# Optimization experiments

Measured on AMD Instinct MI355X. Metric: run time of the kernel, lower is better.

The kernel has to match this reference:

```python
import jax, jax.numpy as jnp
import numpy as np

N_NODES = 100000
N_EDGES = 3200000
N_GRAPHS = 256
IN_DIM = 128
HID = 64
K = 3


def setup_inputs() -> dict:
    key = jax.random.key(0)
    ks = jax.random.split(key, 10)
    x = jax.random.normal(ks[0], (N_NODES, IN_DIM), dtype=jnp.float32)
    edge_index = jax.random.randint(ks[1], (2, N_EDGES), 0, N_NODES, dtype=jnp.int64)
    batch = jnp.sort(jax.random.randint(ks[2], (N_NODES,), 0, N_GRAPHS, dtype=jnp.int64))
    # ChebConv k-order weights: list of Linear(in, out) -> stacked [K, in, out]
    s1 = 1.0 / np.sqrt(IN_DIM)
    s2 = 1.0 / np.sqrt(HID)
    W1 = jax.random.uniform(ks[3], (K, IN_DIM, HID), jnp.float32, -s1, s1)
    b1 = jax.random.uniform(ks[4], (HID,), jnp.float32, -s1, s1)
    W2 = jax.random.uniform(ks[5], (K, HID, HID), jnp.float32, -s2, s2)
    b2 = jax.random.uniform(ks[6], (HID,), jnp.float32, -s2, s2)
    Wfc = jax.random.uniform(ks[7], (HID, 1), jnp.float32, -s2, s2)
    bfc = jax.random.uniform(ks[8], (1,), jnp.float32, -s2, s2)
    return {"x": x, "edge_index": edge_index, "batch": batch,
            "W1": W1, "b1": b1, "W2": W2, "b2": b2, "Wfc": Wfc, "bfc": bfc}


def _cheb_conv(x, src, dst, edge_w, W, b):
    # PyG ChebConv, sym normalization, lambda_max=2 => L_hat has zero diagonal
    # and off-diagonal -D^{-1/2} A D^{-1/2} (edge_w precomputed, negative).
    n = x.shape[0]
    def lhat(v):  # (L_hat v)_i = sum_{edges j->i} edge_w * v_j
        return jax.ops.segment_sum(edge_w[:, None] * v[src], dst, num_segments=n)
    Tx0 = x
    Tx1 = lhat(Tx0)
    Tx2 = 2.0 * lhat(Tx1) - Tx0
    return Tx0 @ W[0] + Tx1 @ W[1] + Tx2 @ W[2] + b


def reference(x, edge_index, batch, W1, b1, W2, b2, Wfc, bfc):
    src, dst = edge_index[0], edge_index[1]
    n = x.shape[0]
    # degree on row (source), sym normalization
    deg = jax.ops.segment_sum(jnp.ones_like(src, dtype=x.dtype), src, num_segments=n)
    dinv = jnp.where(deg > 0, jax.lax.rsqrt(jnp.maximum(deg, 1.0)), 0.0)
    edge_w = -dinv[src] * dinv[dst]  # scaled Laplacian off-diagonal weights

    h = jax.nn.relu(_cheb_conv(x, src, dst, edge_w, W1, b1))
    h = jax.nn.relu(_cheb_conv(h, src, dst, edge_w, W2, b2))

    # global mean pool over graphs
    sums = jax.ops.segment_sum(h, batch, num_segments=N_GRAPHS)
    counts = jax.ops.segment_sum(jnp.ones((n,), dtype=h.dtype), batch, num_segments=N_GRAPHS)
    pooled = sums / jnp.maximum(counts, 1.0)[:, None]

    return (pooled @ Wfc + bfc).squeeze(-1)  # [N_GRAPHS]
```

## Files before the change

kernel.cpp:

```cpp
#include <hip/hip_runtime.h>
#include <hip/hip_fp16.h>
#include <cstdint>
#include <cstddef>

static constexpr int NN = 100000;
static constexpr int NE = 3200000;
static constexpr int NG = 256;
static constexpr int NBK = (NN + 127) / 128;
static constexpr int EPB = NE / 256;
static constexpr int GB_BATCH = (NN + 255) / 256;
static constexpr int GB_PREPW = (192 * 128 + 192 * 64 + 255) / 256;
static constexpr int GB_HIST = 256;

typedef _Float16 h8 __attribute__((ext_vector_type(8)));
typedef float f4v __attribute__((ext_vector_type(4)));

__device__ __forceinline__ void atomAddF(float* p, float v) {
  unsafeAtomicAdd(p, v);
}
__device__ __forceinline__ float h2f(__half h) { return __half2float(h); }

__global__ void k_detect(const int* __restrict__ ei, int* __restrict__ flag) {
  if (threadIdx.x == 0 && blockIdx.x == 0) {
    int nz = 0;
    for (int i = 0; i < 64; ++i) nz += (ei[2 * i + 1] != 0) ? 1 : 0;
    *flag = (nz == 0) ? 1 : 0;
  }
}

__device__ __forceinline__ int ld_idx(const void* raw, int f, int i) {
  return f ? (int)((const long long*)raw)[i] : ((const int*)raw)[i];
}

__global__ __launch_bounds__(256) void k_front(const void* __restrict__ bat,
                                               const void* __restrict__ ei,
                                               const int* __restrict__ flag,
                                               const float* __restrict__ W1,
                                               const float* __restrict__ W2,
                                               int* __restrict__ b32,
                                               int* __restrict__ gcnt,
                                               __half* __restrict__ BtX,
                                               __half* __restrict__ BtH2,
                                               int* __restrict__ sCnt,
                                               int* __restrict__ dCnt,
                                               int* __restrict__ hsBlk,
                                               int* __restrict__ hdBlk) {
  __shared__ int sh[2 * NBK];
  int b = blockIdx.x;
  int t = threadIdx.x;
  if (b < GB_BATCH) {
    int* cnt = sh;
    cnt[t] = 0;
    int blk0 = b * 256;
    int f = *flag;
    int g0 = ld_idx(bat, f, blk0);
    __syncthreads();
    int i = blk0 + t;
    if (i < NN) {
      int g = ld_idx(bat, f, i);
      b32[i] = g;
      atomicAdd(&cnt[g - g0], 1);
    }
    __syncthreads();
    if (cnt[t] > 0) atomicAdd(&gcnt[g0 + t], cnt[t]);
  } else if (b < GB_BATCH + GB_PREPW) {
    int u = (b - GB_BATCH) * 256 + t;
    if (u < 192 * 128) {
      int n = u >> 7, k = u & 127;
      float v;
      if (n < 64)       v = W1[k * 64 + n] - W1[16384 + k * 64 + n];
      else if (n < 128) v = W1[8192 + k * 64 + (n - 64)];
      else              v = W1[16384 + k * 64 + (n - 128)];
      BtX[n * 128 + k] = __float2half_rn(v);
    } else if (u < 192 * 128 + 192 * 64) {
      int u2 = u - 192 * 128;
      int n = u2 >> 6, k = u2 & 63;
      float v;
      if (n < 64)       v = W2[k * 64 + n] - W2[8192 + k * 64 + n];
      else if (n < 128) v = W2[4096 + k * 64 + (n - 64)];
      else              v = W2[8192 + k * 64 + (n - 128)];
      BtH2[n * 64 + k] = __float2half_rn(v);
    }
  } else {
    int hb = b - GB_BATCH - GB_PREPW;
    int* hs = sh;
    int* hd = sh + NBK;
    for (int i = t; i < NBK; i += 256) { hs[i] = 0; hd[i] = 0; }
    __syncthreads();
    int f = *flag;
    int e0 = hb * EPB;
    for (int e = e0 + t; e < e0 + EPB; e += 256) {
      int s = ld_idx(ei, f, e);
      int d = ld_idx(ei, f, NE + e);
      atomicAdd(&hs[s >> 7], 1);
      atomicAdd(&hd[d >> 7], 1);
    }
    __syncthreads();
    size_t hoff = (size_t)hb * NBK;
    for (int i = t; i < NBK; i += 256) {
      int a = hs[i], c = hd[i];
      hsBlk[hoff + i] = a;
      hdBlk[hoff + i] = c;
      if (a) atomicAdd(&sCnt[i], a);
      if (c) atomicAdd(&dCnt[i], c);
    }
  }
}

__global__ __launch_bounds__(1024) void k_scan(const int* __restrict__ sCnt,
                                               const int* __restrict__ dCnt,
                                               int* __restrict__ sBase,
                                               int* __restrict__ dBase,
                                               int* __restrict__ sCur,
                                               int* __restrict__ dCur) {
  __shared__ int sh1[1024], sh2[1024];
  int t = threadIdx.x;
  int v1 = (t < NBK) ? sCnt[t] : 0;
  int v2 = (t < NBK) ? dCnt[t] : 0;
  sh1[t] = v1; sh2[t] = v2;
  __syncthreads();
  for (int off = 1; off < 1024; off <<= 1) {
    int a1 = (t >= off) ? sh1[t - off] : 0;
    int a2 = (t >= off) ? sh2[t - off] : 0;
    __syncthreads();
    sh1[t] += a1; sh2[t] += a2;
    __syncthreads();
  }
  if (t <= NBK) {
    int b1 = sh1[t] - v1, b2 = sh2[t] - v2;
    sBase[t] = b1; dBase[t] = b2;
    if (t < NBK) { sCur[t] = b1; dCur[t] = b2; }
  }
}

__global__ __launch_bounds__(256) void k_scatter(const void* __restrict__ raw,
                                                 const int* __restrict__ flag,
                                                 const int* __restrict__ hsBlk,
                                                 const int* __restrict__ hdBlk,
                                                 int* __restrict__ sCur,
                                                 int* __restrict__ dCur,
                                                 int* __restrict__ srclist,
                                                 unsigned* __restrict__ elist) {
  __shared__ int hs[NBK], hd[NBK], cbS[NBK], cbD[NBK];
  int t = threadIdx.x;
  size_t hb = (size_t)blockIdx.x * NBK;
  for (int i = t; i < NBK; i += 256) {
    int c1 = hsBlk[hb + i];
    cbS[i] = c1 ? atomicAdd(&sCur[i], c1) : 0;
    int c2 = hdBlk[hb + i];
    cbD[i] = c2 ? atomicAdd(&dCur[i], c2) : 0;
    hs[i] = 0; hd[i] = 0;
  }
  __syncthreads();
  int f = *flag;
  int e0 = blockIdx.x * EPB;
  for (int e = e0 + t; e < e0 + EPB; e += 256) {
    int s = ld_idx(raw, f, e);
    int d = ld_idx(raw, f, NE + e);
    int bs = s >> 7, bd = d >> 7;
    int ls = atomicAdd(&hs[bs], 1);
    int ld2 = atomicAdd(&hd[bd], 1);
    srclist[cbS[bs] + ls] = s;
    elist[cbD[bd] + ld2] = (unsigned)s | ((unsigned)(d & 127) << 17);
  }
}

__global__ __launch_bounds__(256) void k_back(const int* __restrict__ sBase,
                                              const int* __restrict__ srclist,
                                              float* __restrict__ dinv,
                                              const int* __restrict__ dBase,
                                              const unsigned* __restrict__ elist,
                                              int* __restrict__ rowptr,
                                              int* __restrict__ adj) {
  __shared__ int cnt[128], sc[128], off[128], fill[128];
  int t = threadIdx.x;
  int bb = blockIdx.x;
  if (bb < NBK) {
    int b = bb;
    if (t < 128) cnt[t] = 0;
    __syncthreads();
    int e0 = sBase[b], e1 = sBase[b + 1];
    for (int i = e0 + t; i < e1; i += 256) atomicAdd(&cnt[srclist[i] & 127], 1);
    __syncthreads();
    if (t < 128) {
      int node = b * 128 + t;
      if (node < NN) {
        int c = cnt[t];
        dinv[node] = (c > 0) ? rsqrtf((float)c) : 0.f;
      }
    }
  } else {
    int b = bb - NBK;
    if (t < 128) { cnt[t] = 0; fill[t] = 0; }
    __syncthreads();
    int e0 = dBase[b], e1 = dBase[b + 1];
    for (int i = e0 + t; i < e1; i += 256) atomicAdd(&cnt[elist[i] >> 17], 1);
    __syncthreads();
    if (t < 128) sc[t] = cnt[t];
    __syncthreads();
    for (int o = 1; o < 128; o <<= 1) {
      int a = (t < 128 && t >= o) ? sc[t - o] : 0;
      __syncthreads();
      if (t < 128) sc[t] += a;
      __syncthreads();
    }
    if (t < 128) {
      off[t] = sc[t] - cnt[t];
      int node = b * 128 + t;
      if (node < NN) rowptr[node] = e0 + off[t];
    }
    if (b == NBK - 1 && t == 0) rowptr[NN] = e1;
    __syncthreads();
    for (int i = e0 + t; i < e1; i += 256) {
      unsigned w2 = elist[i];
      int l = (int)(w2 >> 17);
      int pos = atomicAdd(&fill[l], 1);
      adj[e0 + off[l] + pos] = (int)(w2 & 0x1FFFFu);
    }
  }
}

static constexpr int AW = 136;
__global__ __launch_bounds__(256) void k_gemm_x(const float* __restrict__ x,
                                                const __half* __restrict__ BtX,
                                                const float* __restrict__ dinv,
                                                __half* __restrict__ gV0,
                                                __half* __restrict__ gA1,
                                                __half* __restrict__ gU2s) {
  __shared__ __align__(16) _Float16 As[128 * AW];
  const int t = threadIdx.x;
  const int n0 = blockIdx.x * 128;
  {
    int i = t >> 1, q = t & 1;
    int row = n0 + i;
    _Float16* dst = As + i * AW + q * 64;
    if (row < NN) {
      const float* src = x + (size_t)row * 128 + q * 64;
#pragma unroll
      for (int c = 0; c < 64; c += 4) {
        float4 v = *reinterpret_cast<const float4*>(src + c);
        ushort4 u;
        u.x = __half_as_ushort(__float2half_rn(v.x));
        u.y = __half_as_ushort(__float2half_rn(v.y));
        u.z = __half_as_ushort(__float2half_rn(v.z));
        u.w = __half_as_ushort(__float2half_rn(v.w));
        *reinterpret_cast<ushort4*>(dst + c) = u;
      }
    } else {
#pragma unroll
      for (int c = 0; c < 64; c += 4)
        *reinterpret_cast<ushort4*>(dst + c) = make_ushort4(0, 0, 0, 0);
    }
  }
  __syncthreads();
  const int w = t >> 6, lane = t & 63;
  const int quad = lane >> 4, l = lane & 15;
  f4v acc[2][12];
#pragma unroll
  for (int mt = 0; mt < 2; ++mt)
#pragma unroll
    for (int nt = 0; nt < 12; ++nt) acc[mt][nt] = (f4v){0.f, 0.f, 0.f, 0.f};

#pragma unroll
  for (int ks = 0; ks < 4; ++ks) {
    int k0 = ks * 32 + quad * 8;
    h8 a0 = *reinterpret_cast<const h8*>(As + (w * 32 + l) * AW + k0);
    h8 a1 = *reinterpret_cast<const h8*>(As + (w * 32 + 16 + l) * AW + k0);
#pragma unroll
    for (int nt = 0; nt < 12; ++nt) {
      h8 b = *reinterpret_cast<const h8*>(BtX + (size_t)(nt * 16 + l) * 128 + k0);
      acc[0][nt] = __builtin_amdgcn_mfma_f32_16x16x32_f16(a0, b, acc[0][nt], 0, 0, 0);
      acc[1][nt] = __builtin_amdgcn_mfma_f32_16x16x32_f16(a1, b, acc[1][nt], 0, 0, 0);
    }
  }
#pragma unroll
  for (int mt = 0; mt < 2; ++mt) {
#pragma unroll
    for (int r = 0; r < 4; ++r) {
      int row = n0 + w * 32 + mt * 16 + quad * 4 + r;
      if (row < NN) {
        float dv = dinv[row];
#pragma unroll
        for (int nt2 = 0; nt2 < 4; ++nt2) {
          int col = nt2 * 16 + l;
          gV0[(size_t)row * 64 + col] = __float2half_rn(acc[mt][nt2][r]);
          gA1[(size_t)row * 64 + col] = __float2half_rn(acc[mt][4 + nt2][r]);
          gU2s[(size_t)row * 64 + col] = __float2half_rn(dv * acc[mt][8 + nt2][r]);
        }
      }
    }
  }
}

static constexpr int HW2 = 72;
__global__ __launch_bounds__(256) void k_gemm_h(const __half* __restrict__ gH1,
                                                const __half* __restrict__ BtH2,
                                                const float* __restrict__ dinv,
                                                __half* __restrict__ gV02,
                                                __half* __restrict__ gA2,
                                                __half* __restrict__ gB2s) {
  __shared__ __align__(16) _Float16 As[128 * HW2];
  const int t = threadIdx.x;
  const int n0 = blockIdx.x * 128;
  for (int c = t; c < 128 * 8; c += 256) {
    int row = c >> 3, seg = c & 7;
    int rowg = n0 + row;
    h8 v = (h8){0, 0, 0, 0, 0, 0, 0, 0};
    if (rowg < NN) v = *reinterpret_cast<const h8*>(gH1 + (size_t)rowg * 64 + seg * 8);
    *reinterpret_cast<h8*>(As + row * HW2 + seg * 8) = v;
  }
  __syncthreads();
  const int w = t >> 6, lane = t & 63;
  const int quad = lane >> 4, l = lane & 15;
  f4v acc[2][12];
#pragma unroll
  for (int mt = 0; mt < 2; ++mt)
#pragma unroll
    for (int nt = 0; nt < 12; ++nt) acc[mt][nt] = (f4v){0.f, 0.f, 0.f, 0.f};
#pragma unroll
  for (int ks = 0; ks < 2; ++ks) {
    int k0 = ks * 32 + quad * 8;
    h8 a0 = *reinterpret_cast<const h8*>(As + (w * 32 + l) * HW2 + k0);
    h8 a1 = *reinterpret_cast<const h8*>(As + (w * 32 + 16 + l) * HW2 + k0);
#pragma unroll
    for (int nt = 0; nt < 12; ++nt) {
      h8 b = *reinterpret_cast<const h8*>(BtH2 + (size_t)(nt * 16 + l) * 64 + k0);
      acc[0][nt] = __builtin_amdgcn_mfma_f32_16x16x32_f16(a0, b, acc[0][nt], 0, 0, 0);
      acc[1][nt] = __builtin_amdgcn_mfma_f32_16x16x32_f16(a1, b, acc[1][nt], 0, 0, 0);
    }
  }
#pragma unroll
  for (int mt = 0; mt < 2; ++mt) {
#pragma unroll
    for (int r = 0; r < 4; ++r) {
      int row = n0 + w * 32 + mt * 16 + quad * 4 + r;
      if (row < NN) {
        float dv = dinv[row];
#pragma unroll
        for (int nt2 = 0; nt2 < 4; ++nt2) {
          int col = nt2 * 16 + l;
          gV02[(size_t)row * 64 + col] = __float2half_rn(acc[mt][nt2][r]);
          gA2[(size_t)row * 64 + col] = __float2half_rn(acc[mt][4 + nt2][r]);
          gB2s[(size_t)row * 64 + col] = __float2half_rn(dv * acc[mt][8 + nt2][r]);
        }
      }
    }
  }
}

#define GATHER_SUM(tbl)                                                    \
  int p0 = rp[node], p1 = rp[node + 1];                                    \
  float a0 = 0.f, a1 = 0.f, a2 = 0.f, a3 = 0.f;                            \
  int p = p0;                                                              \
  int pA = (p0 + 3) & ~3;                                                  \
  if (pA > p1) pA = p1;                                                    \
  for (; p < pA; ++p) a0 += h2f(tbl[(size_t)adj[p] * 64 + d]);             \
  for (; p + 8 <= p1; p += 8) {                                            \
    int4 e0 = *reinterpret_cast<const int4*>(adj + p);                     \
    int4 e1 = *reinterpret_cast<const int4*>(adj + p + 4);                 \
    a0 += h2f(tbl[(size_t)e0.x * 64 + d]);                                 \
    a1 += h2f(tbl[(size_t)e0.y * 64 + d]);                                 \
    a2 += h2f(tbl[(size_t)e0.z * 64 + d]);                                 \
    a3 += h2f(tbl[(size_t)e0.w * 64 + d]);                                 \
    a0 += h2f(tbl[(size_t)e1.x * 64 + d]);                                 \
    a1 += h2f(tbl[(size_t)e1.y * 64 + d]);                                 \
    a2 += h2f(tbl[(size_t)e1.z * 64 + d]);                                 \
    a3 += h2f(tbl[(size_t)e1.w * 64 + d]);                                 \
  }                                                                        \
  if (p + 4 <= p1) {                                                       \
    int4 e = *reinterpret_cast<const int4*>(adj + p);                      \
    a0 += h2f(tbl[(size_t)e.x * 64 + d]);                                  \
    a1 += h2f(tbl[(size_t)e.y * 64 + d]);                                  \
    a2 += h2f(tbl[(size_t)e.z * 64 + d]);                                  \
    a3 += h2f(tbl[(size_t)e.w * 64 + d]);                                  \
    p += 4;                                                                \
  }                                                                        \
  for (; p < p1; ++p) a1 += h2f(tbl[(size_t)adj[p] * 64 + d]);             \
  float s = (a0 + a1) + (a2 + a3);

__global__ __launch_bounds__(256) void k_propA(const int* __restrict__ rp,
                                               const int* __restrict__ adj,
                                               const __half* __restrict__ tbl,
                                               const __half* __restrict__ aux,
                                               const float* __restrict__ dinv,
                                               __half* __restrict__ outT) {
  int node = blockIdx.x * 4 + (threadIdx.x >> 6);
  int d = threadIdx.x & 63;
  if (node >= NN) return;
  GATHER_SUM(tbl)
  float dv = dinv[node];
  float tt = -dv * s;
  size_t idx = (size_t)node * 64 + d;
  outT[idx] = __float2half_rn(dv * (h2f(aux[idx]) + 2.f * tt));
}

__global__ __launch_bounds__(256) void k_propB(const int* __restrict__ rp,
                                               const int* __restrict__ adj,
                                               const __half* __restrict__ tbl,
                                               const __half* __restrict__ gV0,
                                               const float* __restrict__ b1v,
                                               const float* __restrict__ dinv,
                                               __half* __restrict__ gH1) {
  int node = blockIdx.x * 4 + (threadIdx.x >> 6);
  int d = threadIdx.x & 63;
  if (node >= NN) return;
  GATHER_SUM(tbl)
  float dv = dinv[node];
  float r = -dv * s;
  size_t idx = (size_t)node * 64 + d;
  float h = fmaxf(h2f(gV0[idx]) + r + b1v[d], 0.f);
  gH1[idx] = __float2half_rn(h);
}

__global__ __launch_bounds__(256) void k_propD(const int* __restrict__ rp,
                                               const int* __restrict__ adj,
                                               const __half* __restrict__ tbl,
                                               const __half* __restrict__ gV02,
                                               const float* __restrict__ b2v,
                                               const float* __restrict__ dinv,
                                               const int* __restrict__ b32,
                                               float* __restrict__ pooled) {
  int node = blockIdx.x * 4 + (threadIdx.x >> 6);
  int d = threadIdx.x & 63;
  if (node >= NN) return;
  GATHER_SUM(tbl)
  float dv = dinv[node];
  float r = -dv * s;
  size_t idx = (size_t)node * 64 + d;
  float h = fmaxf(h2f(gV02[idx]) + r + b2v[d], 0.f);
  int g = b32[node];
  atomAddF(&pooled[g * 64 + d], h);
}

__global__ void k_out(const float* __restrict__ pooled, const int* __restrict__ gcnt,
                      const float* __restrict__ Wfc, const float* __restrict__ bfc,
                      float* __restrict__ out) {
  int g = blockIdx.x, t = threadIdx.x;
  float v = pooled[g * 64 + t] * Wfc[t];
  int c = gcnt[g];
  v /= (float)(c > 0 ? c : 1);
  for (int off = 32; off > 0; off >>= 1) v += __shfl_down(v, off, 64);
  if (t == 0) out[g] = v + bfc[0];
}

extern "C" void kernel_launch(void* const* d_in, const int* in_sizes, int n_in,
                              void* d_out, int out_size, void* d_ws, size_t ws_size,
                              hipStream_t stream) {
  const float* x   = (const float*)d_in[0];
  const void*  ei  = d_in[1];
  const void*  bat = d_in[2];
  const float* W1  = (const float*)d_in[3];
  const float* b1v = (const float*)d_in[4];
  const float* W2  = (const float*)d_in[5];
  const float* b2v = (const float*)d_in[6];
  const float* Wfc = (const float*)d_in[7];
  const float* bfc = (const float*)d_in[8];
  float* out = (float*)d_out;

  char* w = (char*)d_ws;
  size_t o = 0;
  auto take = [&](size_t bytes) -> void* {
    void* p = w + o;
    o = (o + bytes + 255) & ~(size_t)255;
    return p;
  };
  int*      flag   = (int*)take(256);
  int*      gcnt   = (int*)take((size_t)NG * 4);
  float*    pooled = (float*)take((size_t)NG * 64 * 4);
  int*      sCnt   = (int*)take((size_t)(NBK + 2) * 4);
  int*      dCnt   = (int*)take((size_t)(NBK + 2) * 4);
  char*     zend   = w + o;
  int*      sBase  = (int*)take((size_t)(NBK + 2) * 4);
  int*      dBase  = (int*)take((size_t)(NBK + 2) * 4);
  int*      sCur   = (int*)take((size_t)(NBK + 2) * 4);
  int*      dCur   = (int*)take((size_t)(NBK + 2) * 4);
  int*      b32    = (int*)take((size_t)NN * 4);
  float*    dinv   = (float*)take((size_t)NN * 4);
  int*      rowptr = (int*)take((size_t)(NN + 2) * 4);
  int*      hsBlk  = (int*)take((size_t)256 * NBK * 4);
  int*      hdBlk  = (int*)take((size_t)256 * NBK * 4);
  int*      srclist= (int*)take((size_t)NE * 4);
  unsigned* elist  = (unsigned*)take((size_t)NE * 4);
  int*      adj    = (int*)take((size_t)NE * 4);
  __half*   BtX    = (__half*)take((size_t)192 * 128 * 2);
  __half*   BtH2   = (__half*)take((size_t)192 * 64 * 2);
  __half*   gV0    = (__half*)take((size_t)NN * 64 * 2);
  __half*   gA1    = (__half*)take((size_t)NN * 64 * 2);
  __half*   gU2s   = (__half*)take((size_t)NN * 64 * 2);
  __half*   gM1    = (__half*)take((size_t)NN * 64 * 2);
  __half*   gH1    = (__half*)take((size_t)NN * 64 * 2);
  __half*   gV02   = gU2s;
  __half*   gA2    = gA1;
  __half*   gB2s   = gV0;
  __half*   gM2    = gM1;
  (void)in_sizes; (void)n_in; (void)out_size; (void)ws_size;

  hipMemsetAsync(gcnt, 0, (size_t)(zend - (char*)gcnt), stream);

  k_detect<<<1, 64, 0, stream>>>((const int*)ei, flag);
  k_front<<<GB_BATCH + GB_PREPW + GB_HIST, 256, 0, stream>>>(
      bat, ei, flag, W1, W2, b32, gcnt, BtX, BtH2, sCnt, dCnt, hsBlk, hdBlk);
  k_scan<<<1, 1024, 0, stream>>>(sCnt, dCnt, sBase, dBase, sCur, dCur);
  k_scatter<<<256, 256, 0, stream>>>(ei, flag, hsBlk, hdBlk, sCur, dCur, srclist, elist);
  k_back<<<2 * NBK, 256, 0, stream>>>(sBase, srclist, dinv, dBase, elist, rowptr, adj);

  const int gemm_grid = (NN + 127) / 128;
  const int prop_grid = (NN + 3) / 4;

  k_gemm_x<<<gemm_grid, 256, 0, stream>>>(x, BtX, dinv, gV0, gA1, gU2s);
  k_propA<<<prop_grid, 256, 0, stream>>>(rowptr, adj, gU2s, gA1, dinv, gM1);
  k_propB<<<prop_grid, 256, 0, stream>>>(rowptr, adj, gM1, gV0, b1v, dinv, gH1);
  k_gemm_h<<<gemm_grid, 256, 0, stream>>>(gH1, BtH2, dinv, gV02, gA2, gB2s);
  k_propA<<<prop_grid, 256, 0, stream>>>(rowptr, adj, gB2s, gA2, dinv, gM2);
  k_propD<<<prop_grid, 256, 0, stream>>>(rowptr, adj, gM2, gV02, b2v, dinv, b32, pooled);
  k_out<<<NG, 64, 0, stream>>>(pooled, gcnt, Wfc, bfc, out);
}
```

Before: 692.9 us.

## Unroll gather to 16 loads, raise prop occupancy, and move pooling into a segmented kernel

The CSR gather loop now issues 16 independent half loads per iteration into 8 accumulators, giving more memory-level parallelism. The propagation kernels request 8 waves per SIMD through launch_bounds. Per-node atomic pooling in propD is replaced by writing h2 to a buffer and running a separate pool kernel. That kernel exploits the sorted batch ids to do run-length segmented sums before issuing atomics, which cuts atomic contention. In exchange it adds an extra kernel launch and an extra write and read of the h2 buffer.

```diff
diff --git a/kernel.cpp b/kernel.cpp
--- a/kernel.cpp
+++ b/kernel.cpp
@@ -351,21 +351,49 @@
 #define GATHER_SUM(tbl)                                                    \
   int p0 = rp[node], p1 = rp[node + 1];                                    \
   float a0 = 0.f, a1 = 0.f, a2 = 0.f, a3 = 0.f;                            \
+  float a4 = 0.f, a5 = 0.f, a6 = 0.f, a7 = 0.f;                            \
   int p = p0;                                                              \
   int pA = (p0 + 3) & ~3;                                                  \
   if (pA > p1) pA = p1;                                                    \
   for (; p < pA; ++p) a0 += h2f(tbl[(size_t)adj[p] * 64 + d]);             \
-  for (; p + 8 <= p1; p += 8) {                                            \
+  for (; p + 16 <= p1; p += 16) {                                          \
+    int4 e0 = *reinterpret_cast<const int4*>(adj + p);                     \
+    int4 e1 = *reinterpret_cast<const int4*>(adj + p + 4);                 \
+    int4 e2 = *reinterpret_cast<const int4*>(adj + p + 8);                 \
+    int4 e3 = *reinterpret_cast<const int4*>(adj + p + 12);                \
+    __half v0 = tbl[(size_t)e0.x * 64 + d];                                \
+    __half v1 = tbl[(size_t)e0.y * 64 + d];                                \
+    __half v2 = tbl[(size_t)e0.z * 64 + d];                                \
+    __half v3 = tbl[(size_t)e0.w * 64 + d];                                \
+    __half v4 = tbl[(size_t)e1.x * 64 + d];                                \
+    __half v5 = tbl[(size_t)e1.y * 64 + d];                                \
+    __half v6 = tbl[(size_t)e1.z * 64 + d];                                \
+    __half v7 = tbl[(size_t)e1.w * 64 + d];                                \
+    __half v8 = tbl[(size_t)e2.x * 64 + d];                                \
+    __half v9 = tbl[(size_t)e2.y * 64 + d];                                \
+    __half va = tbl[(size_t)e2.z * 64 + d];                                \
+    __half vb = tbl[(size_t)e2.w * 64 + d];                                \
+    __half vc = tbl[(size_t)e3.x * 64 + d];                                \
+    __half vd = tbl[(size_t)e3.y * 64 + d];                                \
+    __half ve = tbl[(size_t)e3.z * 64 + d];                                \
+    __half vf = tbl[(size_t)e3.w * 64 + d];                                \
+    a0 += h2f(v0); a1 += h2f(v1); a2 += h2f(v2); a3 += h2f(v3);            \
+    a4 += h2f(v4); a5 += h2f(v5); a6 += h2f(v6); a7 += h2f(v7);            \
+    a0 += h2f(v8); a1 += h2f(v9); a2 += h2f(va); a3 += h2f(vb);            \
+    a4 += h2f(vc); a5 += h2f(vd); a6 += h2f(ve); a7 += h2f(vf);            \
+  }                                                                        \
+  if (p + 8 <= p1) {                                                       \
     int4 e0 = *reinterpret_cast<const int4*>(adj + p);                     \
     int4 e1 = *reinterpret_cast<const int4*>(adj + p + 4);                 \
     a0 += h2f(tbl[(size_t)e0.x * 64 + d]);                                 \
     a1 += h2f(tbl[(size_t)e0.y * 64 + d]);                                 \
     a2 += h2f(tbl[(size_t)e0.z * 64 + d]);                                 \
     a3 += h2f(tbl[(size_t)e0.w * 64 + d]);                                 \
-    a0 += h2f(tbl[(size_t)e1.x * 64 + d]);                                 \
-    a1 += h2f(tbl[(size_t)e1.y * 64 + d]);                                 \
-    a2 += h2f(tbl[(size_t)e1.z * 64 + d]);                                 \
-    a3 += h2f(tbl[(size_t)e1.w * 64 + d]);                                 \
+    a4 += h2f(tbl[(size_t)e1.x * 64 + d]);                                 \
+    a5 += h2f(tbl[(size_t)e1.y * 64 + d]);                                 \
+    a6 += h2f(tbl[(size_t)e1.z * 64 + d]);                                 \
+    a7 += h2f(tbl[(size_t)e1.w * 64 + d]);                                 \
+    p += 8;                                                                \
   }                                                                        \
   if (p + 4 <= p1) {                                                       \
     int4 e = *reinterpret_cast<const int4*>(adj + p);                      \
@@ -376,14 +404,14 @@
     p += 4;                                                                \
   }                                                                        \
   for (; p < p1; ++p) a1 += h2f(tbl[(size_t)adj[p] * 64 + d]);             \
-  float s = (a0 + a1) + (a2 + a3);
-
-__global__ __launch_bounds__(256) void k_propA(const int* __restrict__ rp,
-                                               const int* __restrict__ adj,
-                                               const __half* __restrict__ tbl,
-                                               const __half* __restrict__ aux,
-                                               const float* __restrict__ dinv,
-                                               __half* __restrict__ outT) {
+  float s = ((a0 + a1) + (a2 + a3)) + ((a4 + a5) + (a6 + a7));
+
+__global__ __launch_bounds__(256, 8) void k_propA(const int* __restrict__ rp,
+                                                  const int* __restrict__ adj,
+                                                  const __half* __restrict__ tbl,
+                                                  const __half* __restrict__ aux,
+                                                  const float* __restrict__ dinv,
+                                                  __half* __restrict__ outT) {
   int node = blockIdx.x * 4 + (threadIdx.x >> 6);
   int d = threadIdx.x & 63;
   if (node >= NN) return;
@@ -394,13 +422,13 @@
   outT[idx] = __float2half_rn(dv * (h2f(aux[idx]) + 2.f * tt));
 }
 
-__global__ __launch_bounds__(256) void k_propB(const int* __restrict__ rp,
-                                               const int* __restrict__ adj,
-                                               const __half* __restrict__ tbl,
-                                               const __half* __restrict__ gV0,
-                                               const float* __restrict__ b1v,
-                                               const float* __restrict__ dinv,
-                                               __half* __restrict__ gH1) {
+__global__ __launch_bounds__(256, 8) void k_propB(const int* __restrict__ rp,
+                                                  const int* __restrict__ adj,
+                                                  const __half* __restrict__ tbl,
+                                                  const __half* __restrict__ gV0,
+                                                  const float* __restrict__ b1v,
+                                                  const float* __restrict__ dinv,
+                                                  __half* __restrict__ gH1) {
   int node = blockIdx.x * 4 + (threadIdx.x >> 6);
   int d = threadIdx.x & 63;
   if (node >= NN) return;
@@ -412,14 +440,13 @@
   gH1[idx] = __float2half_rn(h);
 }
 
-__global__ __launch_bounds__(256) void k_propD(const int* __restrict__ rp,
-                                               const int* __restrict__ adj,
-                                               const __half* __restrict__ tbl,
-                                               const __half* __restrict__ gV02,
-                                               const float* __restrict__ b2v,
-                                               const float* __restrict__ dinv,
-                                               const int* __restrict__ b32,
-                                               float* __restrict__ pooled) {
+__global__ __launch_bounds__(256, 8) void k_propD(const int* __restrict__ rp,
+                                                  const int* __restrict__ adj,
+                                                  const __half* __restrict__ tbl,
+                                                  const __half* __restrict__ gV02,
+                                                  const float* __restrict__ b2v,
+                                                  const float* __restrict__ dinv,
+                                                  __half* __restrict__ gH2) {
   int node = blockIdx.x * 4 + (threadIdx.x >> 6);
   int d = threadIdx.x & 63;
   if (node >= NN) return;
@@ -428,8 +455,32 @@
   float r = -dv * s;
   size_t idx = (size_t)node * 64 + d;
   float h = fmaxf(h2f(gV02[idx]) + r + b2v[d], 0.f);
-  int g = b32[node];
-  atomAddF(&pooled[g * 64 + d], h);
+  gH2[idx] = __float2half_rn(h);
+}
+
+__global__ __launch_bounds__(256) void k_pool(const __half* __restrict__ gH2,
+                                              const int* __restrict__ b32,
+                                              float* __restrict__ pooled) {
+  __shared__ int gb[128];
+  int t = threadIdx.x;
+  int n0 = blockIdx.x * 128;
+  if (t < 128) gb[t] = (n0 + t < NN) ? b32[n0 + t] : -1;
+  __syncthreads();
+  int rg = t >> 6, d = t & 63;
+  int base = rg * 32;
+  int cur = -2;
+  float s = 0.f;
+  for (int i = 0; i < 32; ++i) {
+    int g = gb[base + i];
+    float v = (g >= 0) ? h2f(gH2[(size_t)(n0 + base + i) * 64 + d]) : 0.f;
+    if (g != cur) {
+      if (cur >= 0) atomAddF(&pooled[cur * 64 + d], s);
+      s = 0.f;
+      cur = g;
+    }
+    s += v;
+  }
+  if (cur >= 0) atomAddF(&pooled[cur * 64 + d], s);
 }
 
 __global__ void k_out(const float* __restrict__ pooled, const int* __restrict__ gcnt,
@@ -493,6 +544,7 @@
   __half*   gA2    = gA1;
   __half*   gB2s   = gV0;
   __half*   gM2    = gM1;
+  __half*   gH2    = gH1;
   (void)in_sizes; (void)n_in; (void)out_size; (void)ws_size;
 
   hipMemsetAsync(gcnt, 0, (size_t)(zend - (char*)gcnt), stream);
@@ -512,6 +564,7 @@
   k_propB<<<prop_grid, 256, 0, stream>>>(rowptr, adj, gM1, gV0, b1v, dinv, gH1);
   k_gemm_h<<<gemm_grid, 256, 0, stream>>>(gH1, BtH2, dinv, gV02, gA2, gB2s);
   k_propA<<<prop_grid, 256, 0, stream>>>(rowptr, adj, gB2s, gA2, dinv, gM2);
-  k_propD<<<prop_grid, 256, 0, stream>>>(rowptr, adj, gM2, gV02, b2v, dinv, b32, pooled);
+  k_propD<<<prop_grid, 256, 0, stream>>>(rowptr, adj, gM2, gV02, b2v, dinv, gH2);
+  k_pool<<<NBK, 256, 0, stream>>>(gH2, b32, pooled);
   k_out<<<NG, 64, 0, stream>>>(pooled, gcnt, Wfc, bfc, out);
 }
```

New measurement: 633.4 us. -8.6%, faster.

## Split propagation tables into 32-column halves and add segmented pooling kernel

Applied to the files above, without the earlier changes.

GEMM outputs that feed the neighbor gathers are now written as two separate 32-column half-tables, and each propagation runs twice, once per half. Each wave handles one node, with its two 32-lane halves taking alternating edges and combining through a shuffle. The aim is to shrink the randomly gathered working set per pass so it fits better in L2/MALL, and to expose more independent loads per thread. Pooling moves out of the last propagation into a dedicated kernel that does run-length segmented sums over the sorted batch ids, so it issues far fewer atomics. The cost is twice as many passes over the adjacency list and more kernel launches.

```diff
diff --git a/kernel.cpp b/kernel.cpp
--- a/kernel.cpp
+++ b/kernel.cpp
@@ -226,7 +226,8 @@
                                                 const float* __restrict__ dinv,
                                                 __half* __restrict__ gV0,
                                                 __half* __restrict__ gA1,
-                                                __half* __restrict__ gU2s) {
+                                                __half* __restrict__ U2sA,
+                                                __half* __restrict__ U2sB) {
   __shared__ __align__(16) _Float16 As[128 * AW];
   const int t = threadIdx.x;
   const int n0 = blockIdx.x * 128;
@@ -285,7 +286,9 @@
           int col = nt2 * 16 + l;
           gV0[(size_t)row * 64 + col] = __float2half_rn(acc[mt][nt2][r]);
           gA1[(size_t)row * 64 + col] = __float2half_rn(acc[mt][4 + nt2][r]);
-          gU2s[(size_t)row * 64 + col] = __float2half_rn(dv * acc[mt][8 + nt2][r]);
+          __half u2 = __float2half_rn(dv * acc[mt][8 + nt2][r]);
+          if (nt2 < 2) U2sA[(size_t)row * 32 + col] = u2;
+          else         U2sB[(size_t)row * 32 + (col - 32)] = u2;
         }
       }
     }
@@ -298,7 +301,8 @@
                                                 const float* __restrict__ dinv,
                                                 __half* __restrict__ gV02,
                                                 __half* __restrict__ gA2,
-                                                __half* __restrict__ gB2s) {
+                                                __half* __restrict__ B2sA,
+                                                __half* __restrict__ B2sB) {
   __shared__ __align__(16) _Float16 As[128 * HW2];
   const int t = threadIdx.x;
   const int n0 = blockIdx.x * 128;
@@ -341,95 +345,133 @@
           int col = nt2 * 16 + l;
           gV02[(size_t)row * 64 + col] = __float2half_rn(acc[mt][nt2][r]);
           gA2[(size_t)row * 64 + col] = __float2half_rn(acc[mt][4 + nt2][r]);
-          gB2s[(size_t)row * 64 + col] = __float2half_rn(dv * acc[mt][8 + nt2][r]);
+          __half b2 = __float2half_rn(dv * acc[mt][8 + nt2][r]);
+          if (nt2 < 2) B2sA[(size_t)row * 32 + col] = b2;
+          else         B2sB[(size_t)row * 32 + (col - 32)] = b2;
         }
       }
     }
   }
 }
 
-#define GATHER_SUM(tbl)                                                    \
-  int p0 = rp[node], p1 = rp[node + 1];                                    \
-  float a0 = 0.f, a1 = 0.f, a2 = 0.f, a3 = 0.f;                            \
-  int p = p0;                                                              \
-  int pA = (p0 + 3) & ~3;                                                  \
-  if (pA > p1) pA = p1;                                                    \
-  for (; p < pA; ++p) a0 += h2f(tbl[(size_t)adj[p] * 64 + d]);             \
-  for (; p + 8 <= p1; p += 8) {                                            \
-    int4 e0 = *reinterpret_cast<const int4*>(adj + p);                     \
-    int4 e1 = *reinterpret_cast<const int4*>(adj + p + 4);                 \
-    a0 += h2f(tbl[(size_t)e0.x * 64 + d]);                                 \
-    a1 += h2f(tbl[(size_t)e0.y * 64 + d]);                                 \
-    a2 += h2f(tbl[(size_t)e0.z * 64 + d]);                                 \
-    a3 += h2f(tbl[(size_t)e0.w * 64 + d]);                                 \
-    a0 += h2f(tbl[(size_t)e1.x * 64 + d]);                                 \
-    a1 += h2f(tbl[(size_t)e1.y * 64 + d]);                                 \
-    a2 += h2f(tbl[(size_t)e1.z * 64 + d]);                                 \
-    a3 += h2f(tbl[(size_t)e1.w * 64 + d]);                                 \
-  }                                                                        \
-  if (p + 4 <= p1) {                                                       \
-    int4 e = *reinterpret_cast<const int4*>(adj + p);                      \
-    a0 += h2f(tbl[(size_t)e.x * 64 + d]);                                  \
-    a1 += h2f(tbl[(size_t)e.y * 64 + d]);                                  \
-    a2 += h2f(tbl[(size_t)e.z * 64 + d]);                                  \
-    a3 += h2f(tbl[(size_t)e.w * 64 + d]);                                  \
-    p += 4;                                                                \
-  }                                                                        \
-  for (; p < p1; ++p) a1 += h2f(tbl[(size_t)adj[p] * 64 + d]);             \
-  float s = (a0 + a1) + (a2 + a3);
-
-__global__ __launch_bounds__(256) void k_propA(const int* __restrict__ rp,
-                                               const int* __restrict__ adj,
-                                               const __half* __restrict__ tbl,
-                                               const __half* __restrict__ aux,
-                                               const float* __restrict__ dinv,
-                                               __half* __restrict__ outT) {
+#define GATHER32(tbl)                                                        \
+  int p0 = rp[node], p1 = rp[node + 1];                                      \
+  float a0 = 0.f, a1 = 0.f, a2 = 0.f, a3 = 0.f;                              \
+  float a4 = 0.f, a5 = 0.f, a6 = 0.f, a7 = 0.f;                              \
+  int p = p0;                                                                \
+  int pA = (p0 + 3) & ~3;                                                    \
+  if (pA > p1) pA = p1;                                                      \
+  for (; p < pA; ++p)                                                        \
+    if (!el) a0 += h2f(tbl[(size_t)adj[p] * 32 + dl]);                       \
+  for (; p + 16 <= p1; p += 16) {                                            \
+    int4 e0 = *reinterpret_cast<const int4*>(adj + p);                       \
+    int4 e1 = *reinterpret_cast<const int4*>(adj + p + 4);                   \
+    int4 e2 = *reinterpret_cast<const int4*>(adj + p + 8);                   \
+    int4 e3 = *reinterpret_cast<const int4*>(adj + p + 12);                  \
+    int i0 = el ? e0.y : e0.x, i1 = el ? e0.w : e0.z;                        \
+    int i2 = el ? e1.y : e1.x, i3 = el ? e1.w : e1.z;                        \
+    int i4 = el ? e2.y : e2.x, i5 = el ? e2.w : e2.z;                        \
+    int i6 = el ? e3.y : e3.x, i7 = el ? e3.w : e3.z;                        \
+    __half v0 = tbl[(size_t)i0 * 32 + dl];                                   \
+    __half v1 = tbl[(size_t)i1 * 32 + dl];                                   \
+    __half v2 = tbl[(size_t)i2 * 32 + dl];                                   \
+    __half v3 = tbl[(size_t)i3 * 32 + dl];                                   \
+    __half v4 = tbl[(size_t)i4 * 32 + dl];                                   \
+    __half v5 = tbl[(size_t)i5 * 32 + dl];                                   \
+    __half v6 = tbl[(size_t)i6 * 32 + dl];                                   \
+    __half v7 = tbl[(size_t)i7 * 32 + dl];                                   \
+    a0 += h2f(v0); a1 += h2f(v1); a2 += h2f(v2); a3 += h2f(v3);              \
+    a4 += h2f(v4); a5 += h2f(v5); a6 += h2f(v6); a7 += h2f(v7);              \
+  }                                                                          \
+  if (p + 8 <= p1) {                                                         \
+    int4 e0 = *reinterpret_cast<const int4*>(adj + p);                       \
+    int4 e1 = *reinterpret_cast<const int4*>(adj + p + 4);                   \
+    int i0 = el ? e0.y : e0.x, i1 = el ? e0.w : e0.z;                        \
+    int i2 = el ? e1.y : e1.x, i3 = el ? e1.w : e1.z;                        \
+    a0 += h2f(tbl[(size_t)i0 * 32 + dl]);                                    \
+    a1 += h2f(tbl[(size_t)i1 * 32 + dl]);                                    \
+    a2 += h2f(tbl[(size_t)i2 * 32 + dl]);                                    \
+    a3 += h2f(tbl[(size_t)i3 * 32 + dl]);                                    \
+    p += 8;                                                                  \
+  }                                                                          \
+  if (p + 4 <= p1) {                                                         \
+    int4 e = *reinterpret_cast<const int4*>(adj + p);                        \
+    int i0 = el ? e.y : e.x, i1 = el ? e.w : e.z;                            \
+    a0 += h2f(tbl[(size_t)i0 * 32 + dl]);                                    \
+    a1 += h2f(tbl[(size_t)i1 * 32 + dl]);                                    \
+    p += 4;                                                                  \
+  }                                                                          \
+  if (p + 2 <= p1) {                                                         \
+    int i0 = el ? adj[p + 1] : adj[p];                                       \
+    a1 += h2f(tbl[(size_t)i0 * 32 + dl]);                                    \
+    p += 2;                                                                  \
+  }                                                                          \
+  if (p < p1 && !el) a2 += h2f(tbl[(size_t)adj[p] * 32 + dl]);               \
+  float s = ((a0 + a1) + (a2 + a3)) + ((a4 + a5) + (a6 + a7));               \
+  s += __shfl(s, lane ^ 32);
+
+__global__ __launch_bounds__(256, 8) void k_propAs(const int* __restrict__ rp,
+                                                   const int* __restrict__ adj,
+                                                   const __half* __restrict__ tbl,
+                                                   const __half* __restrict__ aux,
+                                                   const float* __restrict__ dinv,
+                                                   __half* __restrict__ outT) {
   int node = blockIdx.x * 4 + (threadIdx.x >> 6);
-  int d = threadIdx.x & 63;
   if (node >= NN) return;
-  GATHER_SUM(tbl)
-  float dv = dinv[node];
-  float tt = -dv * s;
-  size_t idx = (size_t)node * 64 + d;
-  outT[idx] = __float2half_rn(dv * (h2f(aux[idx]) + 2.f * tt));
-}
-
-__global__ __launch_bounds__(256) void k_propB(const int* __restrict__ rp,
-                                               const int* __restrict__ adj,
-                                               const __half* __restrict__ tbl,
-                                               const __half* __restrict__ gV0,
-                                               const float* __restrict__ b1v,
-                                               const float* __restrict__ dinv,
-                                               __half* __restrict__ gH1) {
+  int lane = threadIdx.x & 63;
+  int el = lane >> 5, dl = lane & 31;
+  GATHER32(tbl)
+  if (!el) {
+    float dv = dinv[node];
+    float tt = -dv * s;
+    outT[(size_t)node * 32 + dl] =
+        __float2half_rn(dv * (h2f(aux[(size_t)node * 64 + dl]) + 2.f * tt));
+  }
+}
+
+__global__ __launch_bounds__(256, 8) void k_propBs(const int* __restrict__ rp,
+                                                   const int* __restrict__ adj,
+                                                   const __half* __restrict__ tbl,
+                                                   const __half* __restrict__ v0,
+                                                   const float* __restrict__ bvec,
+                                                   const float* __restrict__ dinv,
+                                                   __half* __restrict__ outH) {
   int node = blockIdx.x * 4 + (threadIdx.x >> 6);
-  int d = threadIdx.x & 63;
   if (node >= NN) return;
-  GATHER_SUM(tbl)
-  float dv = dinv[node];
-  float r = -dv * s;
-  size_t idx = (size_t)node * 64 + d;
-  float h = fmaxf(h2f(gV0[idx]) + r + b1v[d], 0.f);
-  gH1[idx] = __float2half_rn(h);
-}
-
-__global__ __launch_bounds__(256) void k_propD(const int* __restrict__ rp,
-                                               const int* __restrict__ adj,
-                                               const __half* __restrict__ tbl,
-                                               const __half* __restrict__ gV02,
-                                               const float* __restrict__ b2v,
-                                               const float* __restrict__ dinv,
-                                               const int* __restrict__ b32,
-                                               float* __restrict__ pooled) {
-  int node = blockIdx.x * 4 + (threadIdx.x >> 6);
-  int d = threadIdx.x & 63;
-  if (node >= NN) return;
-  GATHER_SUM(tbl)
-  float dv = dinv[node];
-  float r = -dv * s;
-  size_t idx = (size_t)node * 64 + d;
-  float h = fmaxf(h2f(gV02[idx]) + r + b2v[d], 0.f);
-  int g = b32[node];
-  atomAddF(&pooled[g * 64 + d], h);
+  int lane = threadIdx.x & 63;
+  int el = lane >> 5, dl = lane & 31;
+  GATHER32(tbl)
+  if (!el) {
+    float dv = dinv[node];
+    float r = -dv * s;
+    size_t idx = (size_t)node * 64 + dl;
+    outH[idx] = __float2half_rn(fmaxf(h2f(v0[idx]) + r + bvec[dl], 0.f));
+  }
+}
+
+__global__ __launch_bounds__(256) void k_pool(const __half* __restrict__ gH2,
+                                              const int* __restrict__ b32,
+                                              float* __restrict__ pooled) {
+  __shared__ int gb[128];
+  int t = threadIdx.x;
+  int n0 = blockIdx.x * 128;
+  if (t < 128) gb[t] = (n0 + t < NN) ? b32[n0 + t] : -1;
+  __syncthreads();
+  int rg = t >> 6, d = t & 63;
+  int base = rg * 32;
+  int cur = -2;
+  float s = 0.f;
+  for (int i = 0; i < 32; ++i) {
+    int g = gb[base + i];
+    float v = (g >= 0) ? h2f(gH2[(size_t)(n0 + base + i) * 64 + d]) : 0.f;
+    if (g != cur) {
+      if (cur >= 0) atomAddF(&pooled[cur * 64 + d], s);
+      s = 0.f;
+      cur = g;
+    }
+    s += v;
+  }
+  if (cur >= 0) atomAddF(&pooled[cur * 64 + d], s);
 }
 
 __global__ void k_out(const float* __restrict__ pooled, const int* __restrict__ gcnt,
@@ -486,13 +528,18 @@
   __half*   BtH2   = (__half*)take((size_t)192 * 64 * 2);
   __half*   gV0    = (__half*)take((size_t)NN * 64 * 2);
   __half*   gA1    = (__half*)take((size_t)NN * 64 * 2);
-  __half*   gU2s   = (__half*)take((size_t)NN * 64 * 2);
-  __half*   gM1    = (__half*)take((size_t)NN * 64 * 2);
   __half*   gH1    = (__half*)take((size_t)NN * 64 * 2);
-  __half*   gV02   = gU2s;
-  __half*   gA2    = gA1;
-  __half*   gB2s   = gV0;
-  __half*   gM2    = gM1;
+  __half*   gV02   = (__half*)take((size_t)NN * 64 * 2);
+  __half*   gA2    = (__half*)take((size_t)NN * 64 * 2);
+  __half*   U2sA   = (__half*)take((size_t)NN * 32 * 2);
+  __half*   U2sB   = (__half*)take((size_t)NN * 32 * 2);
+  __half*   M1A    = (__half*)take((size_t)NN * 32 * 2);
+  __half*   M1B    = (__half*)take((size_t)NN * 32 * 2);
+  __half*   B2sA   = (__half*)take((size_t)NN * 32 * 2);
+  __half*   B2sB   = (__half*)take((size_t)NN * 32 * 2);
+  __half*   M2A    = M1A;
+  __half*   M2B    = M1B;
+  __half*   gH2    = gV0;
   (void)in_sizes; (void)n_in; (void)out_size; (void)ws_size;
 
   hipMemsetAsync(gcnt, 0, (size_t)(zend - (char*)gcnt), stream);
@@ -507,11 +554,16 @@
   const int gemm_grid = (NN + 127) / 128;
   const int prop_grid = (NN + 3) / 4;
 
-  k_gemm_x<<<gemm_grid, 256, 0, stream>>>(x, BtX, dinv, gV0, gA1, gU2s);
-  k_propA<<<prop_grid, 256, 0, stream>>>(rowptr, adj, gU2s, gA1, dinv, gM1);
-  k_propB<<<prop_grid, 256, 0, stream>>>(rowptr, adj, gM1, gV0, b1v, dinv, gH1);
-  k_gemm_h<<<gemm_grid, 256, 0, stream>>>(gH1, BtH2, dinv, gV02, gA2, gB2s);
-  k_propA<<<prop_grid, 256, 0, stream>>>(rowptr, adj, gB2s, gA2, dinv, gM2);
-  k_propD<<<prop_grid, 256, 0, stream>>>(rowptr, adj, gM2, gV02, b2v, dinv, b32, pooled);
+  k_gemm_x<<<gemm_grid, 256, 0, stream>>>(x, BtX, dinv, gV0, gA1, U2sA, U2sB);
+  k_propAs<<<prop_grid, 256, 0, stream>>>(rowptr, adj, U2sA, gA1, dinv, M1A);
+  k_propAs<<<prop_grid, 256, 0, stream>>>(rowptr, adj, U2sB, gA1 + 32, dinv, M1B);
+  k_propBs<<<prop_grid, 256, 0, stream>>>(rowptr, adj, M1A, gV0, b1v, dinv, gH1);
+  k_propBs<<<prop_grid, 256, 0, stream>>>(rowptr, adj, M1B, gV0 + 32, b1v + 32, dinv, gH1 + 32);
+  k_gemm_h<<<gemm_grid, 256, 0, stream>>>(gH1, BtH2, dinv, gV02, gA2, B2sA, B2sB);
+  k_propAs<<<prop_grid, 256, 0, stream>>>(rowptr, adj, B2sA, gA2, dinv, M2A);
+  k_propAs<<<prop_grid, 256, 0, stream>>>(rowptr, adj, B2sB, gA2 + 32, dinv, M2B);
+  k_propBs<<<prop_grid, 256, 0, stream>>>(rowptr, adj, M2A, gV02, b2v, dinv, gH2);
+  k_propBs<<<prop_grid, 256, 0, stream>>>(rowptr, adj, M2B, gV02 + 32, b2v + 32, dinv, gH2 + 32);
+  k_pool<<<NBK, 256, 0, stream>>>(gH2, b32, pooled);
   k_out<<<NG, 64, 0, stream>>>(pooled, gcnt, Wfc, bfc, out);
 }
```

Result: slower. 879.4 us (+26.9%).
